# Optimization experiments

Measured on AMD Instinct MI355X. Metric: run time of the kernel, lower is better.

Reference implementation:

```python
import jax, jax.numpy as jnp
import numpy as np

INPUT_SIZE, HIDDEN_SIZE, OUTPUT_SIZE = 256, 512, 256
BATCH, SEQ_LEN = 64, 1024


def _xavier(key, shape):
    fan_out, fan_in = shape
    limit = float(np.sqrt(6.0 / (fan_in + fan_out)))
    return jax.random.uniform(key, shape, jnp.float32, -limit, limit)


def setup_inputs() -> dict:
    key = jax.random.key(0)
    k_x, k_w1, k_w2 = jax.random.split(key, 3)
    x = jax.random.normal(k_x, (BATCH, SEQ_LEN, INPUT_SIZE), jnp.float32)
    W_ih = _xavier(k_w1, (HIDDEN_SIZE, INPUT_SIZE + HIDDEN_SIZE))  # torch Linear weight [out, in]
    b_ih = jnp.zeros((HIDDEN_SIZE,), jnp.float32)
    W_ho = _xavier(k_w2, (OUTPUT_SIZE, HIDDEN_SIZE))
    b_ho = jnp.zeros((OUTPUT_SIZE,), jnp.float32)
    return {"x": x, "W_ih": W_ih, "b_ih": b_ih, "W_ho": W_ho, "b_ho": b_ho}


def reference(x, W_ih, b_ih, W_ho, b_ho):
    batch, seq_len, input_size = x.shape
    hidden = W_ih.shape[0]
    # Split concat-linear into two matmuls: [x_t, h] @ W^T = x_t @ Wx^T + h @ Wh^T
    Wx = W_ih[:, :input_size]   # [H, I]
    Wh = W_ih[:, input_size:]   # [H, H]
    # Precompute input projections for all timesteps: [S, B, H]
    x_proj = jnp.einsum('bsi,hi->sbh', x, Wx) + b_ih

    def step(h, xp_t):
        h_new = jnp.tanh(xp_t + h @ Wh.T)
        return h_new, h_new

    h0 = jnp.zeros((batch, hidden), x.dtype)
    _, hs = jax.lax.scan(step, h0, x_proj)          # hs: [S, B, H]
    hidden_seq = jnp.transpose(hs, (1, 0, 2))       # [B, S, H]
    final_hidden = hidden_seq[:, -1, :]             # [B, H]
    scores = jnp.einsum('bsh,bh->bs', hidden_seq, final_hidden)
    attn = jax.nn.softmax(scores, axis=1)
    context = jnp.einsum('bs,bsh->bh', attn, hidden_seq)
    return context @ W_ho.T + b_ho
```

## Files before the change

kernel.cpp:

```cpp
#include <hip/hip_runtime.h>
#include <cstdint>
#include <cmath>

#define S_LEN 1024
#define BATCH 64
#define IN_SZ 256
#define HID 512
#define OUT_SZ 256
#define WIH_LD 768
#define BH (BATCH * HID)
#define XP_FLOATS (S_LEN * BH)

#define P_REG 176
#define P_LDS 24
#define P_STR_G 14


typedef _Float16 h2v __attribute__((ext_vector_type(2)));
typedef _Float16 f16x8 __attribute__((ext_vector_type(8)));
typedef float f32x4 __attribute__((ext_vector_type(4)));

__device__ __forceinline__ float dot2p(unsigned int a, unsigned int b, float c) {
#if __has_builtin(__builtin_amdgcn_fdot2)
    return __builtin_amdgcn_fdot2(__builtin_bit_cast(h2v, a),
                                  __builtin_bit_cast(h2v, b), c, false);
#else
    h2v av = __builtin_bit_cast(h2v, a);
    h2v bv = __builtin_bit_cast(h2v, b);
    return c + (float)av.x * (float)bv.x + (float)av.y * (float)bv.y;
#endif
}

__device__ __forceinline__ float fast_tanh(float x) {
    float e = __expf(2.0f * x);
#if __has_builtin(__builtin_amdgcn_rcpf)
    float r = __builtin_amdgcn_rcpf(e + 1.0f);
#else
    float r = 1.0f / (e + 1.0f);
#endif
    return __builtin_fmaf(-2.0f, r, 1.0f);
}

__global__ __launch_bounds__(256) void pack_w(const float* __restrict__ W_ih,
                                              unsigned int* __restrict__ wstr,
                                              unsigned int* __restrict__ wregbuf,
                                              unsigned int* __restrict__ wldsbuf) {
    int idx = blockIdx.x * 256 + threadIdx.x;
    int p = idx & 255;
    int j = idx >> 8;
    const float* src = W_ih + (size_t)j * WIH_LD + IN_SZ + 2 * p;
    unsigned short lo = __builtin_bit_cast(unsigned short, (_Float16)src[0]);
    unsigned short hi = __builtin_bit_cast(unsigned short, (_Float16)src[1]);
    unsigned int u = (unsigned int)lo | ((unsigned int)hi << 16);
    if (p < P_REG) {
        wregbuf[p * 512 + j] = u;
    } else if (p < P_REG + P_LDS) {
        wldsbuf[(p - P_REG) * 512 + j] = u;
    } else {
        int q = p - (P_REG + P_LDS);
        wstr[((q >> 2) * 512 + j) * 4 + (q & 3)] = u;
    }
}

__global__ __launch_bounds__(256) void pack_wf16(const float* __restrict__ W_ih,
                                                 uint4* __restrict__ wpk) {
    int idx = blockIdx.x * 256 + threadIdx.x;
    if (idx >= 16384) return;
    int nt   = idx >> 9;
    int ks   = (idx >> 6) & 7;
    int lane = idx & 63;
    int n  = nt * 16 + (lane & 15);
    int kb = ks * 32 + (lane >> 4) * 8;
    const float* src = W_ih + (size_t)n * WIH_LD + kb;
    union { uint4 u; _Float16 h[8]; } v;
#pragma unroll
    for (int i = 0; i < 8; ++i) v.h[i] = (_Float16)src[i];
    wpk[idx] = v.u;
}

#define AH_LD 264
__global__ __launch_bounds__(256) void xproj_mfma(const float* __restrict__ x,
                                                  const uint4* __restrict__ wpk,
                                                  const float* __restrict__ b_ih,
                                                  float* __restrict__ xp) {
    const int s    = blockIdx.x;
    const int half = blockIdx.y;
    const int tid  = threadIdx.x;
    __shared__ __align__(16) _Float16 Ah[32 * AH_LD];
    __shared__ float bsh[HID];
    bsh[tid] = b_ih[tid];
    bsh[tid + 256] = b_ih[tid + 256];
    {
        int r  = tid >> 3;
        int c0 = (tid & 7) * 32;
        const float4* s4 = (const float4*)(x + ((size_t)(half * 32 + r) * S_LEN + s) * IN_SZ + c0);
        _Float16* dst = &Ah[r * AH_LD + c0];
#pragma unroll
        for (int i = 0; i < 8; ++i) {
            float4 v = s4[i];
            dst[4 * i + 0] = (_Float16)v.x;
            dst[4 * i + 1] = (_Float16)v.y;
            dst[4 * i + 2] = (_Float16)v.z;
            dst[4 * i + 3] = (_Float16)v.w;
        }
    }
    __syncthreads();
    const int lane = tid & 63;
    const int w    = tid >> 6;
    const int mt   = w & 1;
    const int ntb  = (w >> 1) * 16;
    f16x8 areg[8];
#pragma unroll
    for (int ks = 0; ks < 8; ++ks)
        areg[ks] = *(const f16x8*)&Ah[(mt * 16 + (lane & 15)) * AH_LD + ks * 32 + (lane >> 4) * 8];
    const int brow  = half * 32 + mt * 16 + (lane >> 4) * 4;
    const int ncol0 = lane & 15;
    for (int nt2 = 0; nt2 < 16; ++nt2) {
        int nt = ntb + nt2;
        const uint4* bp = wpk + (size_t)nt * 8 * 64 + lane;
        f32x4 acc = {0.f, 0.f, 0.f, 0.f};
#pragma unroll
        for (int ks = 0; ks < 8; ++ks) {
            uint4 bu = bp[ks * 64];
            acc = __builtin_amdgcn_mfma_f32_16x16x32_f16(
                areg[ks], __builtin_bit_cast(f16x8, bu), acc, 0, 0, 0);
        }
        int n = nt * 16 + ncol0;
        float bias = bsh[n];
        float* outp = xp + (size_t)s * BH + (size_t)brow * HID + n;
#pragma unroll
        for (int r = 0; r < 4; ++r) outp[(size_t)r * HID] = acc[r] + bias;
    }
}

__global__ __launch_bounds__(512, 2) void rnn_f16(const unsigned int* __restrict__ wregbuf,
                                                  const unsigned int* __restrict__ wldsbuf,
                                                  const uint4* __restrict__ wstr,
                                                  float* __restrict__ xp) {
    const int b = blockIdx.x;
    const int j = threadIdx.x;

    __shared__ unsigned int wlds[P_LDS * 512];
    __shared__ unsigned short h2u[2][512];

    unsigned int wreg[P_REG];
#pragma unroll
    for (int p = 0; p < P_REG; ++p) wreg[p] = wregbuf[p * 512 + j];

    for (int g = j; g < P_LDS * 512; g += 512) wlds[g] = wldsbuf[g];
    h2u[0][j] = 0;
    __syncthreads();

    float* col = xp + (size_t)b * HID + j;
    for (int s = 0; s < S_LEN; ++s) {
        const unsigned int* hq = (const unsigned int*)h2u[s & 1];
        float xpv = col[(size_t)s * BH];

        uint4 sw[P_STR_G];
#pragma unroll
        for (int g = 0; g < P_STR_G; ++g) sw[g] = wstr[(size_t)g * 512 + j];

        float a0 = 0.f, a1 = 0.f, a2 = 0.f, a3 = 0.f;
#pragma unroll
        for (int p = 0; p < P_REG; p += 4) {
            a0 = dot2p(wreg[p + 0], hq[p + 0], a0);
            a1 = dot2p(wreg[p + 1], hq[p + 1], a1);
            a2 = dot2p(wreg[p + 2], hq[p + 2], a2);
            a3 = dot2p(wreg[p + 3], hq[p + 3], a3);
        }
#pragma unroll
        for (int p = 0; p < P_LDS; p += 4) {
            a0 = dot2p(wlds[(p + 0) * 512 + j], hq[P_REG + p + 0], a0);
            a1 = dot2p(wlds[(p + 1) * 512 + j], hq[P_REG + p + 1], a1);
            a2 = dot2p(wlds[(p + 2) * 512 + j], hq[P_REG + p + 2], a2);
            a3 = dot2p(wlds[(p + 3) * 512 + j], hq[P_REG + p + 3], a3);
        }
#pragma unroll
        for (int g = 0; g < P_STR_G; ++g) {
            int pb = P_REG + P_LDS + 4 * g;
            a0 = dot2p(sw[g].x, hq[pb + 0], a0);
            a1 = dot2p(sw[g].y, hq[pb + 1], a1);
            a2 = dot2p(sw[g].z, hq[pb + 2], a2);
            a3 = dot2p(sw[g].w, hq[pb + 3], a3);
        }

        float v = fast_tanh(((a0 + a1) + (a2 + a3)) + xpv);
        col[(size_t)s * BH] = v;
        h2u[(s + 1) & 1][j] = __builtin_bit_cast(unsigned short, (_Float16)v);
        asm volatile("s_waitcnt lgkmcnt(0)" ::: "memory");
        asm volatile("s_barrier" ::: "memory");
    }
}

__global__ __launch_bounds__(256) void attn_sc(const float* __restrict__ hbuf,
                                               float* __restrict__ sc_g) {
    const int b     = blockIdx.x;
    const int chunk = blockIdx.y;
    const int tid   = threadIdx.x;
    const int lane  = tid & 63;
    const int wv    = tid >> 6;
    __shared__ float fh[HID];
    fh[tid] = hbuf[(size_t)(S_LEN - 1) * BH + (size_t)b * HID + tid];
    fh[tid + 256] = hbuf[(size_t)(S_LEN - 1) * BH + (size_t)b * HID + tid + 256];
    __syncthreads();
    float4 f0 = *(const float4*)&fh[lane * 8];
    float4 f1 = *(const float4*)&fh[lane * 8 + 4];
    for (int i = 0; i < 32; ++i) {
        int s = chunk * 128 + wv * 32 + i;
        const float* hr = hbuf + (size_t)s * BH + (size_t)b * HID + lane * 8;
        float4 a0 = *(const float4*)hr;
        float4 a1 = *(const float4*)(hr + 4);
        float p = a0.x * f0.x + a0.y * f0.y + a0.z * f0.z + a0.w * f0.w +
                  a1.x * f1.x + a1.y * f1.y + a1.z * f1.z + a1.w * f1.w;
#pragma unroll
        for (int off = 32; off; off >>= 1) p += __shfl_down(p, off, 64);
        if (lane == 0) sc_g[(size_t)b * S_LEN + s] = p;
    }
}

__global__ __launch_bounds__(256) void attn_ctx(const float* __restrict__ hbuf,
                                                const float* __restrict__ sc_g,
                                                float* __restrict__ ctx_g) {
    const int b   = blockIdx.x;
    const int hc  = blockIdx.y * 128;
    const int tid = threadIdx.x;
    const int lane = tid & 63;
    const int wv   = tid >> 6;
    __shared__ float sc[S_LEN];
    __shared__ float red[4];
    __shared__ float part[256];
    for (int i = tid; i < S_LEN; i += 256) sc[i] = sc_g[(size_t)b * S_LEN + i];
    __syncthreads();
    float m = -1e30f;
    for (int i = tid; i < S_LEN; i += 256) m = fmaxf(m, sc[i]);
#pragma unroll
    for (int off = 32; off; off >>= 1) m = fmaxf(m, __shfl_down(m, off, 64));
    if (lane == 0) red[wv] = m;
    __syncthreads();
    m = fmaxf(fmaxf(red[0], red[1]), fmaxf(red[2], red[3]));
    float sum = 0.f;
    for (int i = tid; i < S_LEN; i += 256) {
        float e = __expf(sc[i] - m);
        sc[i] = e;
        sum += e;
    }
#pragma unroll
    for (int off = 32; off; off >>= 1) sum += __shfl_down(sum, off, 64);
    __syncthreads();
    if (lane == 0) red[wv] = sum;
    __syncthreads();
    float inv = 1.f / (red[0] + red[1] + red[2] + red[3]);
    const int h  = hc + (tid & 127);
    const int sh = tid >> 7;
    const float* hp = hbuf + (size_t)sh * 512 * BH + (size_t)b * HID + h;
    float c = 0.f;
#pragma unroll 4
    for (int s2 = 0; s2 < 512; ++s2)
        c += sc[sh * 512 + s2] * hp[(size_t)s2 * BH];
    part[tid] = c;
    __syncthreads();
    if (tid < 128) ctx_g[(size_t)b * HID + hc + tid] = (part[tid] + part[tid + 128]) * inv;
}

__global__ __launch_bounds__(256) void attn_fin(const float* __restrict__ ctx_g,
                                                const float* __restrict__ W_ho,
                                                const float* __restrict__ b_ho,
                                                float* __restrict__ out) {
    const int b   = blockIdx.x;
    const int tid = threadIdx.x;
    __shared__ float ctx[HID];
    ctx[tid] = ctx_g[(size_t)b * HID + tid];
    ctx[tid + 256] = ctx_g[(size_t)b * HID + tid + 256];
    __syncthreads();
    float o = b_ho[tid];
    const float* wr = W_ho + (size_t)tid * HID;
#pragma unroll 4
    for (int k = 0; k < HID; ++k) o += wr[k] * ctx[k];
    out[(size_t)b * OUT_SZ + tid] = o;
}

extern "C" void kernel_launch(void* const* d_in, const int* in_sizes, int n_in,
                              void* d_out, int out_size, void* d_ws, size_t ws_size,
                              hipStream_t stream) {
    const float* x    = (const float*)d_in[0];
    const float* W_ih = (const float*)d_in[1];
    const float* b_ih = (const float*)d_in[2];
    const float* W_ho = (const float*)d_in[3];
    const float* b_ho = (const float*)d_in[4];
    float* out = (float*)d_out;
    float* ws  = (float*)d_ws;

    float* xp = ws;
    unsigned int* wbase   = (unsigned int*)(ws + XP_FLOATS);
    unsigned int* wstr    = wbase;
    unsigned int* wregbuf = wbase + 28672;
    unsigned int* wldsbuf = wbase + 28672 + P_REG * 512;
    uint4*        wpk     = (uint4*)(wbase + 131072);
    float*        sc_g    = (float*)wbase;
    float*        ctx_g   = (float*)(wbase + 65536);

    pack_w<<<dim3(512), dim3(256), 0, stream>>>(W_ih, wstr, wregbuf, wldsbuf);
    pack_wf16<<<dim3(64), dim3(256), 0, stream>>>(W_ih, wpk);
    xproj_mfma<<<dim3(1024, 2), dim3(256), 0, stream>>>(x, wpk, b_ih, xp);
    rnn_f16<<<dim3(64), dim3(512), 0, stream>>>(wregbuf, wldsbuf, (const uint4*)wstr, xp);
    attn_sc<<<dim3(64, 8), dim3(256), 0, stream>>>(xp, sc_g);
    attn_ctx<<<dim3(64, 4), dim3(256), 0, stream>>>(xp, sc_g, ctx_g);
    attn_fin<<<dim3(64), dim3(256), 0, stream>>>(ctx_g, W_ho, b_ho, out);
}
```

Baseline: 1.758 ms.

## Split RNN recurrence K across two half-blocks, each thread computing two outputs

Restructures the per-step recurrent matvec so each thread computes two hidden outputs over half of the K dimension. The two halves are combined through an LDS scratch buffer with an extra barrier. Pairing outputs lets each uint4 h load from LDS be reused across two weight rows, cutting LDS read traffic per FMA. Weight packing is rearranged to match the new register, LDS and streamed layouts. In exchange it adds a second barrier per timestep, and half the threads sit idle during the tanh/store phase.

```diff
diff --git a/kernel.cpp b/kernel.cpp
--- a/kernel.cpp
+++ b/kernel.cpp
@@ -11,9 +11,9 @@
 #define BH (BATCH * HID)
 #define XP_FLOATS (S_LEN * BH)
 
-#define P_REG 176
-#define P_LDS 24
-#define P_STR_G 14
+#define GR 22
+#define GL 3
+#define GS 7
 
 
 typedef _Float16 h2v __attribute__((ext_vector_type(2)));
@@ -51,14 +51,22 @@
     const float* src = W_ih + (size_t)j * WIH_LD + IN_SZ + 2 * p;
     unsigned short lo = __builtin_bit_cast(unsigned short, (_Float16)src[0]);
     unsigned short hi = __builtin_bit_cast(unsigned short, (_Float16)src[1]);
-    unsigned int u = (unsigned int)lo | ((unsigned int)hi << 16);
-    if (p < P_REG) {
-        wregbuf[p * 512 + j] = u;
-    } else if (p < P_REG + P_LDS) {
-        wldsbuf[(p - P_REG) * 512 + j] = u;
+    unsigned int u32 = (unsigned int)lo | ((unsigned int)hi << 16);
+    int H  = p >> 7;
+    int q  = p & 127;
+    int g  = q >> 2;
+    int c  = q & 3;
+    int u  = j >> 1;
+    int jj = j & 1;
+    if (g < GR) {
+        wregbuf[(((H * GR + g) * 2 + jj) * 256 + u) * 4 + c] = u32;
+    } else if (g < GR + GL) {
+        int gl = g - GR;
+        wldsbuf[(((H * GL + gl) * 2 + jj) * 256 + u) * 4 + c] = u32;
     } else {
-        int q = p - (P_REG + P_LDS);
-        wstr[((q >> 2) * 512 + j) * 4 + (q & 3)] = u;
+        int gs = g - (GR + GL);
+        int t  = H * 256 + u;
+        wstr[((t * GS + gs) * 2 + jj) * 4 + c] = u32;
     }
 }
 
@@ -133,60 +141,107 @@
     }
 }
 
-__global__ __launch_bounds__(512, 2) void rnn_f16(const unsigned int* __restrict__ wregbuf,
-                                                  const unsigned int* __restrict__ wldsbuf,
+__global__ __launch_bounds__(512, 2) void rnn_f16(const uint4* __restrict__ wregbuf,
+                                                  const uint4* __restrict__ wldsbuf,
                                                   const uint4* __restrict__ wstr,
                                                   float* __restrict__ xp) {
     const int b = blockIdx.x;
-    const int j = threadIdx.x;
-
-    __shared__ unsigned int wlds[P_LDS * 512];
-    __shared__ unsigned short h2u[2][512];
-
-    unsigned int wreg[P_REG];
-#pragma unroll
-    for (int p = 0; p < P_REG; ++p) wreg[p] = wregbuf[p * 512 + j];
-
-    for (int g = j; g < P_LDS * 512; g += 512) wlds[g] = wldsbuf[g];
-    h2u[0][j] = 0;
-    __syncthreads();
-
-    float* col = xp + (size_t)b * HID + j;
+    const int t = threadIdx.x;
+    const int H = t >> 8;
+    const int u = t & 255;
+
+    __shared__ __align__(16) uint4 wlds[(GL * 2 * 2) * 256];
+    __shared__ __align__(16) unsigned int h16[2][256];
+    __shared__ __align__(8)  float2 pscr[256];
+
+    uint4 wrA[GR], wrB[GR];
+    {
+        const uint4* wb = wregbuf + (size_t)H * (GR * 2 * 256) + u;
+#pragma unroll
+        for (int g = 0; g < GR; ++g) {
+            wrA[g] = wb[(g * 2 + 0) * 256];
+            wrB[g] = wb[(g * 2 + 1) * 256];
+        }
+    }
+    for (int i = t; i < (GL * 2 * 2) * 256; i += 512) wlds[i] = wldsbuf[i];
+    if (t < 256) h16[0][t] = 0;
+    __syncthreads();
+
+    const uint4* swp = wstr + (size_t)t * (GS * 2);
+    const uint4* wl  = wlds + (size_t)H * (GL * 2 * 256) + u;
+    float* colx = xp + (size_t)b * HID + 2 * u;
+
     for (int s = 0; s < S_LEN; ++s) {
-        const unsigned int* hq = (const unsigned int*)h2u[s & 1];
-        float xpv = col[(size_t)s * BH];
-
-        uint4 sw[P_STR_G];
-#pragma unroll
-        for (int g = 0; g < P_STR_G; ++g) sw[g] = wstr[(size_t)g * 512 + j];
-
-        float a0 = 0.f, a1 = 0.f, a2 = 0.f, a3 = 0.f;
-#pragma unroll
-        for (int p = 0; p < P_REG; p += 4) {
-            a0 = dot2p(wreg[p + 0], hq[p + 0], a0);
-            a1 = dot2p(wreg[p + 1], hq[p + 1], a1);
-            a2 = dot2p(wreg[p + 2], hq[p + 2], a2);
-            a3 = dot2p(wreg[p + 3], hq[p + 3], a3);
-        }
-#pragma unroll
-        for (int p = 0; p < P_LDS; p += 4) {
-            a0 = dot2p(wlds[(p + 0) * 512 + j], hq[P_REG + p + 0], a0);
-            a1 = dot2p(wlds[(p + 1) * 512 + j], hq[P_REG + p + 1], a1);
-            a2 = dot2p(wlds[(p + 2) * 512 + j], hq[P_REG + p + 2], a2);
-            a3 = dot2p(wlds[(p + 3) * 512 + j], hq[P_REG + p + 3], a3);
-        }
-#pragma unroll
-        for (int g = 0; g < P_STR_G; ++g) {
-            int pb = P_REG + P_LDS + 4 * g;
-            a0 = dot2p(sw[g].x, hq[pb + 0], a0);
-            a1 = dot2p(sw[g].y, hq[pb + 1], a1);
-            a2 = dot2p(sw[g].z, hq[pb + 2], a2);
-            a3 = dot2p(sw[g].w, hq[pb + 3], a3);
-        }
-
-        float v = fast_tanh(((a0 + a1) + (a2 + a3)) + xpv);
-        col[(size_t)s * BH] = v;
-        h2u[(s + 1) & 1][j] = __builtin_bit_cast(unsigned short, (_Float16)v);
+        const uint4* hq4 = (const uint4*)&h16[s & 1][0];
+        const int hb = H * 32;
+
+        float2 xpv; xpv.x = 0.f; xpv.y = 0.f;
+        if (H == 0) xpv = *(const float2*)(colx + (size_t)s * BH);
+
+        uint4 sw[GS * 2];
+#pragma unroll
+        for (int i = 0; i < GS * 2; ++i) sw[i] = swp[i];
+
+        float aA0 = 0.f, aA1 = 0.f, aA2 = 0.f, aA3 = 0.f;
+        float aB0 = 0.f, aB1 = 0.f, aB2 = 0.f, aB3 = 0.f;
+
+#pragma unroll
+        for (int g = 0; g < GR; ++g) {
+            uint4 hh = hq4[hb + g];
+            aA0 = dot2p(wrA[g].x, hh.x, aA0);
+            aA1 = dot2p(wrA[g].y, hh.y, aA1);
+            aA2 = dot2p(wrA[g].z, hh.z, aA2);
+            aA3 = dot2p(wrA[g].w, hh.w, aA3);
+            aB0 = dot2p(wrB[g].x, hh.x, aB0);
+            aB1 = dot2p(wrB[g].y, hh.y, aB1);
+            aB2 = dot2p(wrB[g].z, hh.z, aB2);
+            aB3 = dot2p(wrB[g].w, hh.w, aB3);
+        }
+#pragma unroll
+        for (int gl = 0; gl < GL; ++gl) {
+            uint4 hh = hq4[hb + GR + gl];
+            uint4 wA = wl[(gl * 2 + 0) * 256];
+            uint4 wB = wl[(gl * 2 + 1) * 256];
+            aA0 = dot2p(wA.x, hh.x, aA0);
+            aA1 = dot2p(wA.y, hh.y, aA1);
+            aA2 = dot2p(wA.z, hh.z, aA2);
+            aA3 = dot2p(wA.w, hh.w, aA3);
+            aB0 = dot2p(wB.x, hh.x, aB0);
+            aB1 = dot2p(wB.y, hh.y, aB1);
+            aB2 = dot2p(wB.z, hh.z, aB2);
+            aB3 = dot2p(wB.w, hh.w, aB3);
+        }
+#pragma unroll
+        for (int gs = 0; gs < GS; ++gs) {
+            uint4 hh = hq4[hb + GR + GL + gs];
+            uint4 wA = sw[gs * 2 + 0];
+            uint4 wB = sw[gs * 2 + 1];
+            aA0 = dot2p(wA.x, hh.x, aA0);
+            aA1 = dot2p(wA.y, hh.y, aA1);
+            aA2 = dot2p(wA.z, hh.z, aA2);
+            aA3 = dot2p(wA.w, hh.w, aA3);
+            aB0 = dot2p(wB.x, hh.x, aB0);
+            aB1 = dot2p(wB.y, hh.y, aB1);
+            aB2 = dot2p(wB.z, hh.z, aB2);
+            aB3 = dot2p(wB.w, hh.w, aB3);
+        }
+
+        float pA = (aA0 + aA1) + (aA2 + aA3);
+        float pB = (aB0 + aB1) + (aB2 + aB3);
+        if (H == 1) { float2 pv; pv.x = pA; pv.y = pB; pscr[u] = pv; }
+        asm volatile("s_waitcnt lgkmcnt(0)" ::: "memory");
+        asm volatile("s_barrier" ::: "memory");
+        if (H == 0) {
+            float2 pr = pscr[u];
+            float vA = fast_tanh(pA + pr.x + xpv.x);
+            float vB = fast_tanh(pB + pr.y + xpv.y);
+            float2 v2; v2.x = vA; v2.y = vB;
+            *(float2*)(colx + (size_t)s * BH) = v2;
+            unsigned int pk =
+                (unsigned int)__builtin_bit_cast(unsigned short, (_Float16)vA) |
+                ((unsigned int)__builtin_bit_cast(unsigned short, (_Float16)vB) << 16);
+            h16[(s + 1) & 1][u] = pk;
+        }
         asm volatile("s_waitcnt lgkmcnt(0)" ::: "memory");
         asm volatile("s_barrier" ::: "memory");
     }
@@ -294,7 +349,7 @@
     unsigned int* wbase   = (unsigned int*)(ws + XP_FLOATS);
     unsigned int* wstr    = wbase;
     unsigned int* wregbuf = wbase + 28672;
-    unsigned int* wldsbuf = wbase + 28672 + P_REG * 512;
+    unsigned int* wldsbuf = wbase + 118784;
     uint4*        wpk     = (uint4*)(wbase + 131072);
     float*        sc_g    = (float*)wbase;
     float*        ctx_g   = (float*)(wbase + 65536);
@@ -302,7 +357,9 @@
     pack_w<<<dim3(512), dim3(256), 0, stream>>>(W_ih, wstr, wregbuf, wldsbuf);
     pack_wf16<<<dim3(64), dim3(256), 0, stream>>>(W_ih, wpk);
     xproj_mfma<<<dim3(1024, 2), dim3(256), 0, stream>>>(x, wpk, b_ih, xp);
-    rnn_f16<<<dim3(64), dim3(512), 0, stream>>>(wregbuf, wldsbuf, (const uint4*)wstr, xp);
+    rnn_f16<<<dim3(64), dim3(512), 0, stream>>>((const uint4*)wregbuf,
+                                                (const uint4*)wldsbuf,
+                                                (const uint4*)wstr, xp);
     attn_sc<<<dim3(64, 8), dim3(256), 0, stream>>>(xp, sc_g);
     attn_ctx<<<dim3(64, 4), dim3(256), 0, stream>>>(xp, sc_g, ctx_g);
     attn_fin<<<dim3(64), dim3(256), 0, stream>>>(ctx_g, W_ho, b_ho, out);
```

Result: slower. 2.375 ms (+35.1%).
